# Performance work log

Hardware: AMD Instinct MI355X
Metric: run time of the kernel (lower is better)

The kernel has to match this reference:

```python
import jax, jax.numpy as jnp
import numpy as np

N_EMBED = 2048
NUM_EXPERTS = 64
TOP_K = 8
B, S = 4, 8192


def setup_inputs() -> dict:
    key = jax.random.key(0)
    ks = jax.random.split(key, 8)
    scale = 1.0 / np.sqrt(N_EMBED)
    return {
        "x": jax.random.normal(ks[0], (B, S, N_EMBED), dtype=jnp.float32),
        "eps": jax.random.normal(ks[1], (B, S, NUM_EXPERTS), dtype=jnp.float32),
        "w_router": jax.random.uniform(ks[2], (N_EMBED, NUM_EXPERTS), jnp.float32, -scale, scale),
        "b_router": jax.random.uniform(ks[3], (NUM_EXPERTS,), jnp.float32, -scale, scale),
        "w_noise": jax.random.uniform(ks[4], (N_EMBED, NUM_EXPERTS), jnp.float32, -scale, scale),
        "b_noise": jax.random.uniform(ks[5], (NUM_EXPERTS,), jnp.float32, -scale, scale),
        "w_skip": jax.random.uniform(ks[6], (N_EMBED, 1), jnp.float32, -scale, scale),
        "b_skip": jax.random.uniform(ks[7], (1,), jnp.float32, -scale, scale),
    }


def reference(x, eps, w_router, b_router, w_noise, b_noise, w_skip, b_skip):
    # Router and noise logits: [B, S, E]
    logits = jnp.einsum("bsd,de->bse", x, w_router) + b_router
    noise_logits = jnp.einsum("bsd,de->bse", x, w_noise) + b_noise
    # noisy_logits = logits + randn * softplus(noise_logits); randn passed as eps
    noisy_logits = logits + eps * jax.nn.softplus(noise_logits)
    # top-k + scatter(-inf) + softmax == softmax over top-k values scattered back
    top_vals, indices = jax.lax.top_k(noisy_logits, TOP_K)  # [B,S,K]
    gates = jax.nn.softmax(top_vals, axis=-1)  # [B,S,K]
    onehot = jax.nn.one_hot(indices, NUM_EXPERTS, dtype=x.dtype)  # [B,S,K,E]
    router_output = jnp.einsum("bsk,bske->bse", gates, onehot)  # zeros off top-k
    # Sigmoid skip gate: [B, S, 1]
    skip_prob = jax.nn.sigmoid(jnp.einsum("bsd,do->bso", x, w_skip) + b_skip)
    return router_output, indices, skip_prob
```

## Files before the change

kernel.cpp:

```cpp
#include <hip/hip_runtime.h>
#include <math.h>

#define NTOK   32768
#define D      2048
#define E      64
#define TOPK   8

#define BLOCK  256
#define TM     64
#define BK     32
#define NCHUNK (D / BK)
#define NBLK   (NTOK / TM)

#define WBF_BYTES (NCHUNK * 16384)

#define FLAGS_OFF   WBF_BYTES
#define PART_OFF    (WBF_BYTES + 131072)
#define PART_BYTES  ((size_t)2 * NTOK * 128 * 4)
#define SKIPP_OFF   (PART_OFF + PART_BYTES)
#define SKIPP_BYTES ((size_t)2 * NTOK * 4)
#define WS_NEED     (SKIPP_OFF + SKIPP_BYTES)

#define LG_STR 133
#define SP_OFF  34048
#define SMEM_BYTES 34304

#define TIE_EPS 3e-4f

typedef __bf16 bf16x8 __attribute__((ext_vector_type(8)));
typedef __bf16 bf16x2 __attribute__((ext_vector_type(2)));
typedef float  f32x4  __attribute__((ext_vector_type(4)));

__device__ __forceinline__ unsigned short f2bf_rne(float f) {
    unsigned int u = __float_as_uint(f);
    u += 0x7FFFu + ((u >> 16) & 1u);
    return (unsigned short)(u >> 16);
}

__device__ __forceinline__ void split_pack8(const float* xv, uint4& hv, uint4& lv) {
    unsigned int h[8], l[8];
#pragma unroll
    for (int j = 0; j < 8; ++j) {
        unsigned short hb = f2bf_rne(xv[j]);
        float hf = __uint_as_float(((unsigned int)hb) << 16);
        unsigned short lb = f2bf_rne(xv[j] - hf);
        h[j] = hb; l[j] = lb;
    }
    hv.x = h[0] | (h[1] << 16); hv.y = h[2] | (h[3] << 16);
    hv.z = h[4] | (h[5] << 16); hv.w = h[6] | (h[7] << 16);
    lv.x = l[0] | (l[1] << 16); lv.y = l[2] | (l[3] << 16);
    lv.z = l[4] | (l[5] << 16); lv.w = l[6] | (l[7] << 16);
}

__device__ __forceinline__ unsigned int pk2(float a, float b) {
    bf16x2 p;
    p[0] = (__bf16)a; p[1] = (__bf16)b;
    return __builtin_bit_cast(unsigned int, p);
}
__device__ __forceinline__ void split_pack8_v2(const float* xv, uint4& hv, uint4& lv) {
    unsigned int h[4], l[4];
#pragma unroll
    for (int p = 0; p < 4; ++p) {
        float a = xv[2 * p], b = xv[2 * p + 1];
        unsigned int hu = pk2(a, b);
        float fa = __uint_as_float(hu << 16);
        float fb = __uint_as_float(hu & 0xFFFF0000u);
        h[p] = hu;
        l[p] = pk2(a - fa, b - fb);
    }
    hv.x = h[0]; hv.y = h[1]; hv.z = h[2]; hv.w = h[3];
    lv.x = l[0]; lv.y = l[1]; lv.z = l[2]; lv.w = l[3];
}

__global__ __launch_bounds__(256) void convert_w_kernel(
    const float* __restrict__ wr, const float* __restrict__ wn, char* __restrict__ wbf)
{
    int u = blockIdx.x * 256 + threadIdx.x;
    int col  = u & 127;
    int koct = (u >> 7) & 3;
    int c    = u >> 9;
    const float* src = (col < 64)
        ? (wr + (size_t)(c * BK + koct * 8) * E + col)
        : (wn + (size_t)(c * BK + koct * 8) * E + (col - 64));
    float xv[8];
#pragma unroll
    for (int j = 0; j < 8; ++j) xv[j] = src[(size_t)j * E];
    uint4 hv, lv;
    split_pack8(xv, hv, lv);
    char* dst = wbf + (size_t)c * 16384 + (size_t)(koct * 128 + col) * 16;
    *(uint4*)dst = hv;
    *(uint4*)(dst + 8192) = lv;
}

__global__ __launch_bounds__(BLOCK) void gemm_part_kernel(
    const float* __restrict__ x, const char* __restrict__ wbf,
    const float* __restrict__ w_skip,
    float* __restrict__ part, float* __restrict__ skip_part)
{
    const int tid = threadIdx.x;
    const int kp  = blockIdx.x & 1;
    const int tb  = blockIdx.x >> 1;
    const int tokBase = tb * TM;
    const int c0 = kp * 32;

    const int lane = tid & 63;
    const int wv   = __builtin_amdgcn_readfirstlane(tid >> 6);
    const int tg   = wv >> 1;
    const int ch   = wv & 1;
    const int q    = lane >> 4;
    const int m    = lane & 15;

    const float* xlane  = x + (size_t)(tokBase + tg * 32 + m) * D + q * 8 + (size_t)c0 * BK;
    const char*  blane  = wbf + (size_t)((q << 7) + (ch << 6) + m) * 16 + (size_t)c0 * 16384;
    const float* wklane = w_skip + q * 8 + c0 * BK;

    f32x4 acc[2][4];
#pragma unroll
    for (int tt = 0; tt < 2; ++tt)
#pragma unroll
        for (int cw = 0; cw < 4; ++cw) acc[tt][cw] = (f32x4){0.f, 0.f, 0.f, 0.f};
    float skipAcc[2] = {0.f, 0.f};

    struct Gen {
        float4 a[2][2];
        uint4  b[4][2];
        float4 wk[2];
    };

    auto loadGen = [&](Gen& g, int c) {
        const float* xp = xlane + c * BK;
#pragma unroll
        for (int tt = 0; tt < 2; ++tt) {
            g.a[tt][0] = *(const float4*)(xp + (size_t)tt * 16 * D);
            g.a[tt][1] = *(const float4*)(xp + (size_t)tt * 16 * D + 4);
        }
        const char* bp = blane + (size_t)c * 16384;
#pragma unroll
        for (int cw = 0; cw < 4; ++cw) {
            g.b[cw][0] = *(const uint4*)(bp + cw * 256);
            g.b[cw][1] = *(const uint4*)(bp + cw * 256 + 8192);
        }
        g.wk[0] = *(const float4*)(wklane + c * BK);
        g.wk[1] = *(const float4*)(wklane + c * BK + 4);
    };

    auto computeGen = [&](Gen& g) {
#pragma unroll
        for (int tt = 0; tt < 2; ++tt) {
            float xv[8] = {g.a[tt][0].x, g.a[tt][0].y, g.a[tt][0].z, g.a[tt][0].w,
                           g.a[tt][1].x, g.a[tt][1].y, g.a[tt][1].z, g.a[tt][1].w};
            uint4 hv, lv;
            split_pack8_v2(xv, hv, lv);
            bf16x8 Ah = __builtin_bit_cast(bf16x8, hv);
            bf16x8 Al = __builtin_bit_cast(bf16x8, lv);
#pragma unroll
            for (int cw = 0; cw < 4; ++cw) {
                bf16x8 Bh = __builtin_bit_cast(bf16x8, g.b[cw][0]);
                bf16x8 Bl = __builtin_bit_cast(bf16x8, g.b[cw][1]);
                acc[tt][cw] = __builtin_amdgcn_mfma_f32_16x16x32_bf16(Ah, Bh, acc[tt][cw], 0, 0, 0);
                acc[tt][cw] = __builtin_amdgcn_mfma_f32_16x16x32_bf16(Ah, Bl, acc[tt][cw], 0, 0, 0);
                acc[tt][cw] = __builtin_amdgcn_mfma_f32_16x16x32_bf16(Al, Bh, acc[tt][cw], 0, 0, 0);
            }
            float s = skipAcc[tt];
            s = fmaf(xv[0], g.wk[0].x, s); s = fmaf(xv[1], g.wk[0].y, s);
            s = fmaf(xv[2], g.wk[0].z, s); s = fmaf(xv[3], g.wk[0].w, s);
            s = fmaf(xv[4], g.wk[1].x, s); s = fmaf(xv[5], g.wk[1].y, s);
            s = fmaf(xv[6], g.wk[1].z, s); s = fmaf(xv[7], g.wk[1].w, s);
            skipAcc[tt] = s;
        }
    };

    Gen gA, gB;
    loadGen(gA, 0);
#pragma unroll 1
    for (int c = 0; c < 32; c += 2) {
        loadGen(gB, c + 1);
        computeGen(gA);
        if (c + 2 < 32) loadGen(gA, c + 2);
        computeGen(gB);
    }

    float* pbase = part + (size_t)kp * NTOK * 128 + (size_t)tokBase * 128;
#pragma unroll
    for (int tt = 0; tt < 2; ++tt)
#pragma unroll
        for (int cw = 0; cw < 4; ++cw) {
#pragma unroll
            for (int reg = 0; reg < 4; ++reg) {
                int token = tg * 32 + tt * 16 + q * 4 + reg;
                int col = ch * 64 + cw * 16 + m;
                pbase[(size_t)token * 128 + col] = acc[tt][cw][reg];
            }
        }

#pragma unroll
    for (int tt = 0; tt < 2; ++tt) {
        skipAcc[tt] += __shfl_xor(skipAcc[tt], 16);
        skipAcc[tt] += __shfl_xor(skipAcc[tt], 32);
    }
    if (ch == 0 && lane < 16) {
        float* spg = skip_part + (size_t)kp * NTOK + tokBase + tg * 32;
        spg[lane]      = skipAcc[0];
        spg[16 + lane] = skipAcc[1];
    }
}

__global__ __launch_bounds__(256) void combine_kernel(
    const float* __restrict__ part, const float* __restrict__ skip_part,
    const float* __restrict__ eps,
    const float* __restrict__ b_router, const float* __restrict__ b_noise,
    const float* __restrict__ b_skip,
    float* __restrict__ out_router, float* __restrict__ out_idx,
    float* __restrict__ out_skip, int* __restrict__ flags, int cap)
{
    __shared__ __attribute__((aligned(16))) float lg[TM * LG_STR];
    const int tid = threadIdx.x;
    const int blk = blockIdx.x;
    const int tokBase = blk * TM;

    const float4* p0 = (const float4*)(part + (size_t)blk * TM * 128);
    const float4* p1 = (const float4*)(part + (size_t)NTOK * 128 + (size_t)blk * TM * 128);
#pragma unroll
    for (int r = 0; r < 8; ++r) {
        int j = r * 256 + tid;
        float4 a = p0[j], b = p1[j];
        int tok = j >> 5;
        int col = (j & 31) * 4;
        float* dst = lg + tok * LG_STR + col;
        dst[0] = a.x + b.x; dst[1] = a.y + b.y;
        dst[2] = a.z + b.z; dst[3] = a.w + b.w;
    }
    __syncthreads();

    if (tid < 64) {
        const int t = tid;
        const int tok = tokBase + t;
        float* row = lg + t * LG_STR;

        float sv = skip_part[tok] + skip_part[NTOK + tok] + b_skip[0];
        out_skip[tok] = 1.f / (1.f + expf(-sv));

        const float4* epsr = (const float4*)(eps + (size_t)tok * E);
#pragma unroll 4
        for (int e4 = 0; e4 < 16; ++e4) {
            float4 ep = epsr[e4];
            float epv[4] = {ep.x, ep.y, ep.z, ep.w};
#pragma unroll
            for (int u2 = 0; u2 < 4; ++u2) {
                int e = e4 * 4 + u2;
                float lgv = row[e] + b_router[e];
                float nl  = row[64 + e] + b_noise[e];
                float sp  = fmaxf(nl, 0.f) + log1pf(expf(-fabsf(nl)));
                row[e] = lgv + epv[u2] * sp;
            }
        }

        float vals[9];
        int idxs[8];
        for (int p = 0; p < 9; ++p) {
            float best = -INFINITY;
            int bi = 0;
            for (int e = 0; e < 64; ++e) {
                float v = row[e];
                if (v > best) { best = v; bi = e; }
            }
            vals[p] = best;
            if (p < 8) idxs[p] = bi;
            row[bi] = -INFINITY;
        }

        float mg = 1e30f;
#pragma unroll
        for (int p = 0; p < 8; ++p) mg = fminf(mg, vals[p] - vals[p + 1]);
        if (mg < TIE_EPS) {
            int slot = atomicAdd(flags, 1);
            if (slot < cap) flags[2 + slot] = tok;
        }

        float mx = vals[0];
        float g[8], s = 0.f;
#pragma unroll
        for (int p = 0; p < 8; ++p) { g[p] = expf(vals[p] - mx); s += g[p]; }
        float inv = 1.f / s;

        float* rrow = row + 64;
#pragma unroll
        for (int e = 0; e < 64; ++e) rrow[e] = 0.f;
#pragma unroll
        for (int p = 0; p < 8; ++p) rrow[idxs[p]] = g[p] * inv;
#pragma unroll
        for (int e4 = 0; e4 < 16; ++e4) {
            float4 o = make_float4(rrow[e4 * 4], rrow[e4 * 4 + 1],
                                   rrow[e4 * 4 + 2], rrow[e4 * 4 + 3]);
            *(float4*)(out_router + (size_t)tok * E + e4 * 4) = o;
        }
        float4 i0 = make_float4((float)idxs[0], (float)idxs[1], (float)idxs[2], (float)idxs[3]);
        float4 i1 = make_float4((float)idxs[4], (float)idxs[5], (float)idxs[6], (float)idxs[7]);
        *(float4*)(out_idx + (size_t)tok * TOPK)     = i0;
        *(float4*)(out_idx + (size_t)tok * TOPK + 4) = i1;
    }
}

__global__ __launch_bounds__(BLOCK, 2) void router_kernel(
    const float* __restrict__ x, const float* __restrict__ eps,
    const char* __restrict__ wbf,
    const float* __restrict__ b_router, const float* __restrict__ b_noise,
    const float* __restrict__ w_skip, const float* __restrict__ b_skip,
    float* __restrict__ out_router, float* __restrict__ out_idx,
    float* __restrict__ out_skip, int* __restrict__ flags, int cap)
{
    __shared__ __attribute__((aligned(16))) char smem[SMEM_BYTES];
    const int tid = threadIdx.x;
    const int tokBase = blockIdx.x * TM;

    const int lane = tid & 63;
    const int wv   = __builtin_amdgcn_readfirstlane(tid >> 6);
    const int tg   = wv >> 1;
    const int ch   = wv & 1;
    const int q    = lane >> 4;
    const int m    = lane & 15;

    const float* xlane = x + (size_t)(tokBase + tg * 32 + m) * D + q * 8;
    const char*  blane = wbf + (size_t)((q << 7) + (ch << 6) + m) * 16;
    const float* wklane = w_skip + q * 8;

    f32x4 acc[2][4];
#pragma unroll
    for (int tt = 0; tt < 2; ++tt)
#pragma unroll
        for (int cw = 0; cw < 4; ++cw) acc[tt][cw] = (f32x4){0.f, 0.f, 0.f, 0.f};
    float skipAcc[2] = {0.f, 0.f};

    struct Gen {
        float4 a[2][2];
        uint4  b[4][2];
        float4 wk[2];
    };

    auto loadGen = [&](Gen& g, int c) {
        const float* xp = xlane + c * BK;
#pragma unroll
        for (int tt = 0; tt < 2; ++tt) {
            g.a[tt][0] = *(const float4*)(xp + (size_t)tt * 16 * D);
            g.a[tt][1] = *(const float4*)(xp + (size_t)tt * 16 * D + 4);
        }
        const char* bp = blane + (size_t)c * 16384;
#pragma unroll
        for (int cw = 0; cw < 4; ++cw) {
            g.b[cw][0] = *(const uint4*)(bp + cw * 256);
            g.b[cw][1] = *(const uint4*)(bp + cw * 256 + 8192);
        }
        g.wk[0] = *(const float4*)(wklane + c * BK);
        g.wk[1] = *(const float4*)(wklane + c * BK + 4);
    };

    auto computeGen = [&](Gen& g) {
#pragma unroll
        for (int tt = 0; tt < 2; ++tt) {
            float xv[8] = {g.a[tt][0].x, g.a[tt][0].y, g.a[tt][0].z, g.a[tt][0].w,
                           g.a[tt][1].x, g.a[tt][1].y, g.a[tt][1].z, g.a[tt][1].w};
            uint4 hv, lv;
            split_pack8(xv, hv, lv);
            bf16x8 Ah = __builtin_bit_cast(bf16x8, hv);
            bf16x8 Al = __builtin_bit_cast(bf16x8, lv);
#pragma unroll
            for (int cw = 0; cw < 4; ++cw) {
                bf16x8 Bh = __builtin_bit_cast(bf16x8, g.b[cw][0]);
                bf16x8 Bl = __builtin_bit_cast(bf16x8, g.b[cw][1]);
                acc[tt][cw] = __builtin_amdgcn_mfma_f32_16x16x32_bf16(Ah, Bh, acc[tt][cw], 0, 0, 0);
                acc[tt][cw] = __builtin_amdgcn_mfma_f32_16x16x32_bf16(Ah, Bl, acc[tt][cw], 0, 0, 0);
                acc[tt][cw] = __builtin_amdgcn_mfma_f32_16x16x32_bf16(Al, Bh, acc[tt][cw], 0, 0, 0);
            }
            float s = skipAcc[tt];
            s = fmaf(xv[0], g.wk[0].x, s); s = fmaf(xv[1], g.wk[0].y, s);
            s = fmaf(xv[2], g.wk[0].z, s); s = fmaf(xv[3], g.wk[0].w, s);
            s = fmaf(xv[4], g.wk[1].x, s); s = fmaf(xv[5], g.wk[1].y, s);
            s = fmaf(xv[6], g.wk[1].z, s); s = fmaf(xv[7], g.wk[1].w, s);
            skipAcc[tt] = s;
        }
    };

    Gen gA, gB;
    loadGen(gA, 0);
#pragma unroll 1
    for (int c = 0; c < NCHUNK; c += 2) {
        loadGen(gB, c + 1);
        computeGen(gA);
        if (c + 2 < NCHUNK) loadGen(gA, c + 2);
        computeGen(gB);
    }

    float* lg = (float*)smem;
#pragma unroll
    for (int tt = 0; tt < 2; ++tt)
#pragma unroll
        for (int cw = 0; cw < 4; ++cw) {
#pragma unroll
            for (int reg = 0; reg < 4; ++reg) {
                int token = tg * 32 + tt * 16 + q * 4 + reg;
                int col = ch * 64 + cw * 16 + m;
                lg[token * LG_STR + col] = acc[tt][cw][reg];
            }
        }

#pragma unroll
    for (int tt = 0; tt < 2; ++tt) {
        skipAcc[tt] += __shfl_xor(skipAcc[tt], 16);
        skipAcc[tt] += __shfl_xor(skipAcc[tt], 32);
    }
    if (ch == 0 && lane < 16) {
        float* sp = (float*)(smem + SP_OFF);
        sp[tg * 32 + lane]      = skipAcc[0];
        sp[tg * 32 + 16 + lane] = skipAcc[1];
    }
    __syncthreads();

    if (tid < 64) {
        const int t = tid;
        const int tok = tokBase + t;
        float* row = lg + t * LG_STR;

        float sv = ((float*)(smem + SP_OFF))[t] + b_skip[0];
        out_skip[tok] = 1.f / (1.f + expf(-sv));

        const float4* epsr = (const float4*)(eps + (size_t)tok * E);
#pragma unroll 4
        for (int e4 = 0; e4 < 16; ++e4) {
            float4 ep = epsr[e4];
            float epv[4] = {ep.x, ep.y, ep.z, ep.w};
#pragma unroll
            for (int u2 = 0; u2 < 4; ++u2) {
                int e = e4 * 4 + u2;
                float lgv = row[e] + b_router[e];
                float nl  = row[64 + e] + b_noise[e];
                float sp  = fmaxf(nl, 0.f) + log1pf(expf(-fabsf(nl)));
                row[e] = lgv + epv[u2] * sp;
            }
        }

        float vals[9];
        int idxs[8];
        for (int p = 0; p < 9; ++p) {
            float best = -INFINITY;
            int bi = 0;
            for (int e = 0; e < 64; ++e) {
                float v = row[e];
                if (v > best) { best = v; bi = e; }
            }
            vals[p] = best;
            if (p < 8) idxs[p] = bi;
            row[bi] = -INFINITY;
        }

        float mg = 1e30f;
#pragma unroll
        for (int p = 0; p < 8; ++p) mg = fminf(mg, vals[p] - vals[p + 1]);
        if (mg < TIE_EPS) {
            int slot = atomicAdd(flags, 1);
            if (slot < cap) flags[2 + slot] = tok;
        }

        float mx = vals[0];
        float g[8], s = 0.f;
#pragma unroll
        for (int p = 0; p < 8; ++p) { g[p] = expf(vals[p] - mx); s += g[p]; }
        float inv = 1.f / s;

        float* rrow = row + 64;
#pragma unroll
        for (int e = 0; e < 64; ++e) rrow[e] = 0.f;
#pragma unroll
        for (int p = 0; p < 8; ++p) rrow[idxs[p]] = g[p] * inv;
#pragma unroll
        for (int e4 = 0; e4 < 16; ++e4) {
            float4 o = make_float4(rrow[e4 * 4], rrow[e4 * 4 + 1],
                                   rrow[e4 * 4 + 2], rrow[e4 * 4 + 3]);
            *(float4*)(out_router + (size_t)tok * E + e4 * 4) = o;
        }
        float4 i0 = make_float4((float)idxs[0], (float)idxs[1], (float)idxs[2], (float)idxs[3]);
        float4 i1 = make_float4((float)idxs[4], (float)idxs[5], (float)idxs[6], (float)idxs[7]);
        *(float4*)(out_idx + (size_t)tok * TOPK)     = i0;
        *(float4*)(out_idx + (size_t)tok * TOPK + 4) = i1;
    }
}

__global__ __launch_bounds__(256) void fixup_kernel(
    const float* __restrict__ x, const float* __restrict__ eps,
    const float* __restrict__ w_router, const float* __restrict__ b_router,
    const float* __restrict__ w_noise, const float* __restrict__ b_noise,
    float* __restrict__ out_router, float* __restrict__ out_idx,
    const int* __restrict__ flags, int cap)
{
    __shared__ double smR[4][64];
    __shared__ double smN[4][64];
    __shared__ double noisy[64];
    const int tid  = threadIdx.x;
    const int lane = tid & 63;
    const int qw   = tid >> 6;

    int count = flags[0];
    if (count > cap) count = cap;

    for (int i = blockIdx.x; i < count; i += gridDim.x) {
        int tok = flags[2 + i];
        const float4* xr4 = (const float4*)(x + (size_t)tok * D + qw * 512);
        const float* wrB = w_router + (size_t)(qw * 512) * E + lane;
        const float* wnB = w_noise  + (size_t)(qw * 512) * E + lane;

        double pr0 = 0, pr1 = 0, pr2 = 0, pr3 = 0;
        double pn0 = 0, pn1 = 0, pn2 = 0, pn3 = 0;
#pragma unroll 4
        for (int it = 0; it < 128; ++it) {
            float4 xv = xr4[it];
            const float* wr = wrB + (size_t)(it * 4) * E;
            const float* wn = wnB + (size_t)(it * 4) * E;
            pr0 += (double)xv.x * (double)wr[0];
            pr1 += (double)xv.y * (double)wr[E];
            pr2 += (double)xv.z * (double)wr[2 * E];
            pr3 += (double)xv.w * (double)wr[3 * E];
            pn0 += (double)xv.x * (double)wn[0];
            pn1 += (double)xv.y * (double)wn[E];
            pn2 += (double)xv.z * (double)wn[2 * E];
            pn3 += (double)xv.w * (double)wn[3 * E];
        }
        smR[qw][lane] = (pr0 + pr1) + (pr2 + pr3);
        smN[qw][lane] = (pn0 + pn1) + (pn2 + pn3);
        __syncthreads();

        if (tid < 64) {
            double lgv = smR[0][tid] + smR[1][tid] + smR[2][tid] + smR[3][tid] + (double)b_router[tid];
            double nl  = smN[0][tid] + smN[1][tid] + smN[2][tid] + smN[3][tid] + (double)b_noise[tid];
            double sp  = fmax(nl, 0.0) + log1p(exp(-fabs(nl)));
            noisy[tid] = lgv + (double)eps[(size_t)tok * E + tid] * sp;
        }
        __syncthreads();

        if (tid == 0) {
            double tmp[64];
            for (int j = 0; j < 64; ++j) tmp[j] = noisy[j];
            double vals[8]; int idxs[8];
            for (int p = 0; p < 8; ++p) {
                double best = -1e300; int bi = 0;
                for (int j = 0; j < 64; ++j)
                    if (tmp[j] > best) { best = tmp[j]; bi = j; }
                vals[p] = best; idxs[p] = bi; tmp[bi] = -1e300;
            }
            double mx = vals[0], s = 0.0, g[8];
            for (int p = 0; p < 8; ++p) { g[p] = exp(vals[p] - mx); s += g[p]; }
            float rowv[64];
            for (int j = 0; j < 64; ++j) rowv[j] = 0.f;
            for (int p = 0; p < 8; ++p) rowv[idxs[p]] = (float)(g[p] / s);
            for (int j = 0; j < 64; ++j) out_router[(size_t)tok * E + j] = rowv[j];
            for (int p = 0; p < 8; ++p) out_idx[(size_t)tok * TOPK + p] = (float)idxs[p];
        }
        __syncthreads();
    }
}

extern "C" void kernel_launch(void* const* d_in, const int* in_sizes, int n_in,
                              void* d_out, int out_size, void* d_ws, size_t ws_size,
                              hipStream_t stream) {
    const float* x        = (const float*)d_in[0];
    const float* eps      = (const float*)d_in[1];
    const float* w_router = (const float*)d_in[2];
    const float* b_router = (const float*)d_in[3];
    const float* w_noise  = (const float*)d_in[4];
    const float* b_noise  = (const float*)d_in[5];
    const float* w_skip   = (const float*)d_in[6];
    const float* b_skip   = (const float*)d_in[7];

    float* out = (float*)d_out;
    float* out_router = out;
    float* out_idx    = out + (size_t)NTOK * E;
    float* out_skip   = out_idx + (size_t)NTOK * TOPK;

    char* wbf  = (char*)d_ws;
    int* flags = (int*)((char*)d_ws + FLAGS_OFF);

    convert_w_kernel<<<dim3(128), dim3(256), 0, stream>>>(w_router, w_noise, wbf);

    if (ws_size >= WS_NEED) {
        int cap = 16384;
        hipMemsetAsync((char*)d_ws + FLAGS_OFF, 0, 8, stream);

        float* part      = (float*)((char*)d_ws + PART_OFF);
        float* skip_part = (float*)((char*)d_ws + SKIPP_OFF);

        gemm_part_kernel<<<dim3(2 * NBLK), dim3(BLOCK), 0, stream>>>(
            x, wbf, w_skip, part, skip_part);

        combine_kernel<<<dim3(NBLK), dim3(BLOCK), 0, stream>>>(
            part, skip_part, eps, b_router, b_noise, b_skip,
            out_router, out_idx, out_skip, flags, cap);

        fixup_kernel<<<dim3(8192), dim3(256), 0, stream>>>(
            x, eps, w_router, b_router, w_noise, b_noise,
            out_router, out_idx, flags, cap);
    } else {
        int cap = 0;
        if (ws_size > WBF_BYTES + 16) {
            size_t c = (ws_size - WBF_BYTES - 8) / 4;
            cap = (c > 16384) ? 16384 : (int)c;
        }
        hipMemsetAsync((char*)d_ws + FLAGS_OFF, 0, 8, stream);

        router_kernel<<<dim3(NBLK), dim3(BLOCK), 0, stream>>>(
            x, eps, wbf, b_router, b_noise, w_skip, b_skip,
            out_router, out_idx, out_skip, flags, cap);

        fixup_kernel<<<dim3(8192), dim3(256), 0, stream>>>(
            x, eps, w_router, b_router, w_noise, b_noise,
            out_router, out_idx, flags, cap);
    }
}
```

Baseline: 581.5 us.

## Fuse split-K GEMM and combine via last-arriver atomic pairing

Merges the split-K partial GEMM and the combine/top-k kernel into a single kernel. Each token block's two K-halves increment a per-block atomic counter, and the second block to arrive adds its register accumulators to the other half's partials and runs the softmax/top-k epilogue. This removes one kernel launch and the re-read of its own partials from global memory. In exchange it adds an extra memset, fences and atomics, plus shared-memory use in the GEMM kernel that may lower occupancy.

Result: slower. 708.0 us (+21.8%).

```diff
diff --git a/kernel.cpp b/kernel.cpp
--- a/kernel.cpp
+++ b/kernel.cpp
@@ -15,6 +15,7 @@
 #define WBF_BYTES (NCHUNK * 16384)
 
 #define FLAGS_OFF   WBF_BYTES
+#define PAIR_OFF    (FLAGS_OFF + 65544)
 #define PART_OFF    (WBF_BYTES + 131072)
 #define PART_BYTES  ((size_t)2 * NTOK * 128 * 4)
 #define SKIPP_OFF   (PART_OFF + PART_BYTES)
@@ -92,11 +93,20 @@
     *(uint4*)(dst + 8192) = lv;
 }
 
-__global__ __launch_bounds__(BLOCK) void gemm_part_kernel(
+__global__ __launch_bounds__(BLOCK) void gemm_fused_kernel(
     const float* __restrict__ x, const char* __restrict__ wbf,
-    const float* __restrict__ w_skip,
-    float* __restrict__ part, float* __restrict__ skip_part)
+    const float* __restrict__ w_skip, const float* __restrict__ eps,
+    const float* __restrict__ b_router, const float* __restrict__ b_noise,
+    const float* __restrict__ b_skip,
+    float* __restrict__ part, float* __restrict__ skip_part,
+    float* __restrict__ out_router, float* __restrict__ out_idx,
+    float* __restrict__ out_skip, int* __restrict__ flags,
+    int* __restrict__ pair, int cap)
 {
+    __shared__ __attribute__((aligned(16))) float lg[TM * LG_STR];
+    __shared__ float sps[TM];
+    __shared__ int sOld;
+
     const int tid = threadIdx.x;
     const int kp  = blockIdx.x & 1;
     const int tb  = blockIdx.x >> 1;
@@ -202,34 +212,35 @@
         float* spg = skip_part + (size_t)kp * NTOK + tokBase + tg * 32;
         spg[lane]      = skipAcc[0];
         spg[16 + lane] = skipAcc[1];
-    }
-}
-
-__global__ __launch_bounds__(256) void combine_kernel(
-    const float* __restrict__ part, const float* __restrict__ skip_part,
-    const float* __restrict__ eps,
-    const float* __restrict__ b_router, const float* __restrict__ b_noise,
-    const float* __restrict__ b_skip,
-    float* __restrict__ out_router, float* __restrict__ out_idx,
-    float* __restrict__ out_skip, int* __restrict__ flags, int cap)
-{
-    __shared__ __attribute__((aligned(16))) float lg[TM * LG_STR];
-    const int tid = threadIdx.x;
-    const int blk = blockIdx.x;
-    const int tokBase = blk * TM;
-
-    const float4* p0 = (const float4*)(part + (size_t)blk * TM * 128);
-    const float4* p1 = (const float4*)(part + (size_t)NTOK * 128 + (size_t)blk * TM * 128);
-#pragma unroll
-    for (int r = 0; r < 8; ++r) {
-        int j = r * 256 + tid;
-        float4 a = p0[j], b = p1[j];
-        int tok = j >> 5;
-        int col = (j & 31) * 4;
-        float* dst = lg + tok * LG_STR + col;
-        dst[0] = a.x + b.x; dst[1] = a.y + b.y;
-        dst[2] = a.z + b.z; dst[3] = a.w + b.w;
-    }
+        sps[tg * 32 + lane]      = skipAcc[0];
+        sps[tg * 32 + 16 + lane] = skipAcc[1];
+    }
+    __syncthreads();
+
+    if (tid == 0) {
+        __threadfence();
+        sOld = atomicAdd(&pair[tb], 1);
+    }
+    __syncthreads();
+    if (sOld != 1) return;
+
+    if (tid == 0) __threadfence();
+    __syncthreads();
+
+    const int okp = kp ^ 1;
+    const float* obase = part + (size_t)okp * NTOK * 128 + (size_t)tokBase * 128;
+#pragma unroll
+    for (int tt = 0; tt < 2; ++tt)
+#pragma unroll
+        for (int cw = 0; cw < 4; ++cw) {
+#pragma unroll
+            for (int reg = 0; reg < 4; ++reg) {
+                int token = tg * 32 + tt * 16 + q * 4 + reg;
+                int col = ch * 64 + cw * 16 + m;
+                lg[token * LG_STR + col] =
+                    acc[tt][cw][reg] + obase[(size_t)token * 128 + col];
+            }
+        }
     __syncthreads();
 
     if (tid < 64) {
@@ -237,7 +248,7 @@
         const int tok = tokBase + t;
         float* row = lg + t * LG_STR;
 
-        float sv = skip_part[tok] + skip_part[NTOK + tok] + b_skip[0];
+        float sv = sps[t] + skip_part[(size_t)okp * NTOK + tok] + b_skip[0];
         out_skip[tok] = 1.f / (1.f + expf(-sv));
 
         const float4* epsr = (const float4*)(eps + (size_t)tok * E);
@@ -581,17 +592,16 @@
 
     if (ws_size >= WS_NEED) {
         int cap = 16384;
+        int* pair = (int*)((char*)d_ws + PAIR_OFF);
         hipMemsetAsync((char*)d_ws + FLAGS_OFF, 0, 8, stream);
+        hipMemsetAsync((char*)d_ws + PAIR_OFF, 0, NBLK * sizeof(int), stream);
 
         float* part      = (float*)((char*)d_ws + PART_OFF);
         float* skip_part = (float*)((char*)d_ws + SKIPP_OFF);
 
-        gemm_part_kernel<<<dim3(2 * NBLK), dim3(BLOCK), 0, stream>>>(
-            x, wbf, w_skip, part, skip_part);
-
-        combine_kernel<<<dim3(NBLK), dim3(BLOCK), 0, stream>>>(
-            part, skip_part, eps, b_router, b_noise, b_skip,
-            out_router, out_idx, out_skip, flags, cap);
+        gemm_fused_kernel<<<dim3(2 * NBLK), dim3(BLOCK), 0, stream>>>(
+            x, wbf, w_skip, eps, b_router, b_noise, b_skip,
+            part, skip_part, out_router, out_idx, out_skip, flags, pair, cap);
 
         fixup_kernel<<<dim3(8192), dim3(256), 0, stream>>>(
             x, eps, w_router, b_router, w_noise, b_noise,
```
